# Kernel optimization log

Hardware: AMD Instinct MI355X
Metric: run time of the kernel (lower is better)

Reference implementation:

```python
import jax, jax.numpy as jnp
import numpy as np

B, C, H, W = 2, 512, 48, 48
HEADS = 8
REDUCTION = 4
DPH = max(C // REDUCTION // HEADS, 1)   # 16
TOTAL = DPH * HEADS                      # 128
EPS_NORM = 1e-12
EPS_BN = 1e-5


def setup_inputs() -> dict:
    key = jax.random.key(0)
    ks = jax.random.split(key, 6)
    x = jax.random.normal(ks[0], (B, C, H, W), dtype=jnp.float32)
    # 1x1 convs stored as [out_ch, in_ch] matrices
    w_qkv = jax.random.normal(ks[1], (3 * TOTAL, C), dtype=jnp.float32) * (1.0 / np.sqrt(C))
    w_out = jax.random.normal(ks[2], (C, TOTAL), dtype=jnp.float32) * (1.0 / np.sqrt(TOTAL))
    temperature = jnp.ones((HEADS, 1, 1), dtype=jnp.float32)
    bn_gamma = jnp.ones((C,), dtype=jnp.float32)
    bn_beta = jnp.zeros((C,), dtype=jnp.float32)
    return {"x": x, "w_qkv": w_qkv, "temperature": temperature,
            "w_out": w_out, "bn_gamma": bn_gamma, "bn_beta": bn_beta}


def _l2norm(t):
    # F.normalize(t, dim=-1): t / max(||t||_2, eps)
    n = jnp.sqrt(jnp.sum(t * t, axis=-1, keepdims=True))
    return t / jnp.maximum(n, EPS_NORM)


def reference(x, w_qkv, temperature, w_out, bn_gamma, bn_beta):
    b, c, h, w = x.shape
    n = h * w
    # qkv 1x1 conv: [b, 3*TOTAL, h, w]
    qkv = jnp.einsum('bchw,oc->bohw', x, w_qkv)
    q, k, v = jnp.split(qkv, 3, axis=1)
    # [b, heads, dph, n] -> [b, heads, n, dph]
    def heads_tokens(t):
        return t.reshape(b, HEADS, DPH, n).transpose(0, 1, 3, 2)
    q = _l2norm(heads_tokens(q))
    k = _l2norm(heads_tokens(k))
    v = heads_tokens(v)
    # [b, heads, n, n]
    attn = jnp.einsum('bhnd,bhmd->bhnm', q, k) * temperature[None]
    attn = jax.nn.softmax(attn, axis=-1)
    out = jnp.einsum('bhnm,bhmd->bhnd', attn, v)          # [b, heads, n, dph]
    out = out.transpose(0, 1, 3, 2).reshape(b, TOTAL, h, w)
    # project_out: 1x1 conv then BatchNorm2d (training-mode batch stats)
    out = jnp.einsum('bthw,ct->bchw', out, w_out)
    mean = jnp.mean(out, axis=(0, 2, 3))
    var = jnp.mean((out - mean[None, :, None, None]) ** 2, axis=(0, 2, 3))
    out = (out - mean[None, :, None, None]) * jax.lax.rsqrt(var + EPS_BN)[None, :, None, None]
    out = out * bn_gamma[None, :, None, None] + bn_beta[None, :, None, None]
    return out
```

## Files before the change

kernel.cpp:

```cpp
#include <hip/hip_runtime.h>

#define NB 2
#define CC 512
#define NN 2304
#define NH 8
#define DD 16
#define TT 128
#define O3 384

typedef __attribute__((ext_vector_type(4))) float f32x4;
typedef __attribute__((ext_vector_type(8))) __bf16 bf16x8;
typedef __attribute__((ext_vector_type(4))) __bf16 bf16x4;
typedef __attribute__((ext_vector_type(4))) _Float16 f16x4;
typedef __attribute__((ext_vector_type(2))) __fp16 hf16x2;

union hf2pair {
    hf16x2 h[2];
    f16x4  v;
};

#define OFF_XT 0u
#define OFF_WQ 4718592u
#define OFF_WO 5111808u
#define OFF_Q  5242880u
#define OFF_K  6422528u
#define OFF_VT 7602176u
#define OFF_AO 8781824u
#define OFF_PRE 9961472u

__global__ __launch_bounds__(256) void k0_convert(
    const float* __restrict__ x, const float* __restrict__ wqkv,
    const float* __restrict__ wout,
    __bf16* __restrict__ xT, __bf16* __restrict__ wqb, __bf16* __restrict__ wob)
{
    int bid = blockIdx.x;
    int t = threadIdx.x;
    if (bid < 576) {
        __shared__ float tile[64][65];
        int b = bid / 288, rem = bid % 288;
        int nt = rem / 8, cb = rem % 8;
        int n0 = nt * 64, c0 = cb * 64;
        int tc = t >> 6, tn = t & 63;
#pragma unroll
        for (int i = 0; i < 16; i++) {
            int cl = i * 4 + tc;
            tile[cl][tn] = x[(size_t)(b * CC + c0 + cl) * NN + n0 + tn];
        }
        __syncthreads();
#pragma unroll
        for (int i = 0; i < 16; i++) {
            int nl = i * 4 + tc;
            xT[(size_t)(b * NN + n0 + nl) * CC + c0 + tn] = (__bf16)tile[tn][nl];
        }
    } else {
        int wid = bid - 576;
        int base = wid * 256 + t;
#pragma unroll
        for (int i = 0; i < 16; i++) {
            int j = base + i * 16384;
            if (j < O3 * CC) wqb[j] = (__bf16)wqkv[j];
            else             wob[j - O3 * CC] = (__bf16)wout[j - O3 * CC];
        }
    }
}

__global__ __launch_bounds__(256) void k1_qkv(
    const __bf16* __restrict__ xT, const __bf16* __restrict__ wqb,
    _Float16* __restrict__ Q, _Float16* __restrict__ K, _Float16* __restrict__ VT)
{
    int ob = blockIdx.x, nt = blockIdx.y, b = blockIdx.z;
    int lane = threadIdx.x & 63, wave = threadIdx.x >> 6;
    int quad = lane >> 4, col = lane & 15;
    int n0 = nt * 64 + wave * 16;
    int o0 = ob * 64;

    f32x4 acc0 = {0.f,0.f,0.f,0.f}, acc1 = {0.f,0.f,0.f,0.f};
    f32x4 acc2 = {0.f,0.f,0.f,0.f}, acc3 = {0.f,0.f,0.f,0.f};

    const __bf16* arow  = xT + (size_t)(b * NN + n0 + col) * CC + quad * 8;
    const __bf16* brow0 = wqb + (size_t)(o0 + col) * CC + quad * 8;
    const __bf16* brow1 = brow0 + 16 * CC;
    const __bf16* brow2 = brow0 + 32 * CC;
    const __bf16* brow3 = brow0 + 48 * CC;

    bf16x8 a  = *(const bf16x8*)(arow);
    bf16x8 w0 = *(const bf16x8*)(brow0);
    bf16x8 w1 = *(const bf16x8*)(brow1);
    bf16x8 w2 = *(const bf16x8*)(brow2);
    bf16x8 w3 = *(const bf16x8*)(brow3);
#pragma unroll
    for (int ks = 0; ks < 16; ks++) {
        bf16x8 an, wn0, wn1, wn2, wn3;
        if (ks < 15) {
            an  = *(const bf16x8*)(arow + (ks + 1) * 32);
            wn0 = *(const bf16x8*)(brow0 + (ks + 1) * 32);
            wn1 = *(const bf16x8*)(brow1 + (ks + 1) * 32);
            wn2 = *(const bf16x8*)(brow2 + (ks + 1) * 32);
            wn3 = *(const bf16x8*)(brow3 + (ks + 1) * 32);
        }
        acc0 = __builtin_amdgcn_mfma_f32_16x16x32_bf16(a, w0, acc0, 0, 0, 0);
        acc1 = __builtin_amdgcn_mfma_f32_16x16x32_bf16(a, w1, acc1, 0, 0, 0);
        acc2 = __builtin_amdgcn_mfma_f32_16x16x32_bf16(a, w2, acc2, 0, 0, 0);
        acc3 = __builtin_amdgcn_mfma_f32_16x16x32_bf16(a, w3, acc3, 0, 0, 0);
        a = an; w0 = wn0; w1 = wn1; w2 = wn2; w3 = wn3;
    }

#pragma unroll
    for (int s = 0; s < 4; s++) {
        int oc = o0 + s * 16 + col;
        int d = oc & 15, h = (oc >> 4) & 7, kind = oc >> 7;
        f32x4 v = (s == 0) ? acc0 : (s == 1) ? acc1 : (s == 2) ? acc2 : acc3;
        if (kind < 2) {
            float ss0 = v[0] * v[0], ss1 = v[1] * v[1], ss2 = v[2] * v[2], ss3 = v[3] * v[3];
#pragma unroll
            for (int m = 1; m < 16; m <<= 1) {
                ss0 += __shfl_xor(ss0, m);
                ss1 += __shfl_xor(ss1, m);
                ss2 += __shfl_xor(ss2, m);
                ss3 += __shfl_xor(ss3, m);
            }
            v[0] *= 1.0f / fmaxf(sqrtf(ss0), 1e-12f);
            v[1] *= 1.0f / fmaxf(sqrtf(ss1), 1e-12f);
            v[2] *= 1.0f / fmaxf(sqrtf(ss2), 1e-12f);
            v[3] *= 1.0f / fmaxf(sqrtf(ss3), 1e-12f);
            _Float16* dst = (kind == 0 ? Q : K) + (size_t)(b * NH + h) * NN * DD;
#pragma unroll
            for (int r = 0; r < 4; r++) {
                int n = n0 + quad * 4 + r;
                dst[(size_t)n * DD + d] = (_Float16)v[r];
            }
        } else {
            f16x4 pk;
#pragma unroll
            for (int r = 0; r < 4; r++) pk[r] = (_Float16)v[r];
            int n = n0 + quad * 4;
            *(f16x4*)(VT + (size_t)((b * NH + h) * DD + d) * NN + n) = pk;
        }
    }
}

__global__ __launch_bounds__(512) void k2_attn(
    const _Float16* __restrict__ Q, const _Float16* __restrict__ K,
    const _Float16* __restrict__ VT, const float* __restrict__ temp,
    __bf16* __restrict__ AO)
{
    __shared__ float Osh[8][16][64];
    __shared__ float Lsh[8][64];

    int qt = blockIdx.x, bh = blockIdx.y;
    int lane = threadIdx.x & 63, wave = threadIdx.x >> 6;
    int quad = lane >> 4, col = lane & 15;
    int kbase = wave * 288;
    int qbase = qt * 64;

    const _Float16* Qb = Q + (size_t)bh * NN * DD;
    float tl2 = temp[bh & 7] * 1.4426950408889634f;
    _Float16 tl2h = (_Float16)tl2;

    f16x4 qf0 = *(const f16x4*)(Qb + (size_t)(qbase +  0 + col) * DD + quad * 4);
    f16x4 qf1 = *(const f16x4*)(Qb + (size_t)(qbase + 16 + col) * DD + quad * 4);
    f16x4 qf2 = *(const f16x4*)(Qb + (size_t)(qbase + 32 + col) * DD + quad * 4);
    f16x4 qf3 = *(const f16x4*)(Qb + (size_t)(qbase + 48 + col) * DD + quad * 4);
#pragma unroll
    for (int j = 0; j < 4; j++) {
        qf0[j] *= tl2h; qf1[j] *= tl2h; qf2[j] *= tl2h; qf3[j] *= tl2h;
    }
    const f16x4 onesf = {(_Float16)1.f, (_Float16)1.f, (_Float16)1.f, (_Float16)1.f};

    f32x4 oa0 = {0.f,0.f,0.f,0.f}, oa1 = {0.f,0.f,0.f,0.f};
    f32x4 oa2 = {0.f,0.f,0.f,0.f}, oa3 = {0.f,0.f,0.f,0.f};
    f32x4 lc0 = {0.f,0.f,0.f,0.f}, lc1 = {0.f,0.f,0.f,0.f};
    f32x4 lc2 = {0.f,0.f,0.f,0.f}, lc3 = {0.f,0.f,0.f,0.f};
    const f32x4 zc = {0.f,0.f,0.f,0.f};

    const _Float16* kp = K + (size_t)bh * NN * DD + (size_t)(kbase + col) * DD + quad * 4;
    const _Float16* vp = VT + (size_t)bh * DD * NN + (size_t)col * NN + kbase + quad * 4;

    f16x4 kfa = *(const f16x4*)(kp);
    f16x4 kfb = *(const f16x4*)(kp + 16 * DD);
    f16x4 vfa = *(const f16x4*)(vp);
    f16x4 vfb = *(const f16x4*)(vp + 16);

#define K2_CHUNK(KF, VF)                                                        \
    {                                                                           \
        f32x4 s0 = __builtin_amdgcn_mfma_f32_16x16x16f16(KF, qf0, zc, 0, 0, 0); \
        f32x4 s1 = __builtin_amdgcn_mfma_f32_16x16x16f16(KF, qf1, zc, 0, 0, 0); \
        f32x4 s2 = __builtin_amdgcn_mfma_f32_16x16x16f16(KF, qf2, zc, 0, 0, 0); \
        f32x4 s3 = __builtin_amdgcn_mfma_f32_16x16x16f16(KF, qf3, zc, 0, 0, 0); \
        hf2pair u0, u1, u2, u3;                                                 \
        u0.h[0] = __builtin_amdgcn_cvt_pkrtz(__builtin_amdgcn_exp2f(s0[0]),     \
                                             __builtin_amdgcn_exp2f(s0[1]));    \
        u0.h[1] = __builtin_amdgcn_cvt_pkrtz(__builtin_amdgcn_exp2f(s0[2]),     \
                                             __builtin_amdgcn_exp2f(s0[3]));    \
        u1.h[0] = __builtin_amdgcn_cvt_pkrtz(__builtin_amdgcn_exp2f(s1[0]),     \
                                             __builtin_amdgcn_exp2f(s1[1]));    \
        u1.h[1] = __builtin_amdgcn_cvt_pkrtz(__builtin_amdgcn_exp2f(s1[2]),     \
                                             __builtin_amdgcn_exp2f(s1[3]));    \
        u2.h[0] = __builtin_amdgcn_cvt_pkrtz(__builtin_amdgcn_exp2f(s2[0]),     \
                                             __builtin_amdgcn_exp2f(s2[1]));    \
        u2.h[1] = __builtin_amdgcn_cvt_pkrtz(__builtin_amdgcn_exp2f(s2[2]),     \
                                             __builtin_amdgcn_exp2f(s2[3]));    \
        u3.h[0] = __builtin_amdgcn_cvt_pkrtz(__builtin_amdgcn_exp2f(s3[0]),     \
                                             __builtin_amdgcn_exp2f(s3[1]));    \
        u3.h[1] = __builtin_amdgcn_cvt_pkrtz(__builtin_amdgcn_exp2f(s3[2]),     \
                                             __builtin_amdgcn_exp2f(s3[3]));    \
        f16x4 p0 = u0.v, p1 = u1.v, p2 = u2.v, p3 = u3.v;                       \
        lc0 = __builtin_amdgcn_mfma_f32_16x16x16f16(onesf, p0, lc0, 0, 0, 0);   \
        lc1 = __builtin_amdgcn_mfma_f32_16x16x16f16(onesf, p1, lc1, 0, 0, 0);   \
        lc2 = __builtin_amdgcn_mfma_f32_16x16x16f16(onesf, p2, lc2, 0, 0, 0);   \
        lc3 = __builtin_amdgcn_mfma_f32_16x16x16f16(onesf, p3, lc3, 0, 0, 0);   \
        oa0 = __builtin_amdgcn_mfma_f32_16x16x16f16(VF, p0, oa0, 0, 0, 0);      \
        oa1 = __builtin_amdgcn_mfma_f32_16x16x16f16(VF, p1, oa1, 0, 0, 0);      \
        oa2 = __builtin_amdgcn_mfma_f32_16x16x16f16(VF, p2, oa2, 0, 0, 0);      \
        oa3 = __builtin_amdgcn_mfma_f32_16x16x16f16(VF, p3, oa3, 0, 0, 0);      \
    }

    for (int g = 0; g < 9; ++g) {
        f16x4 kna, knb, vna, vnb;
        if (g < 8) {
            kna = *(const f16x4*)(kp + 32 * DD);
            knb = *(const f16x4*)(kp + 48 * DD);
            vna = *(const f16x4*)(vp + 32);
            vnb = *(const f16x4*)(vp + 48);
        }
        K2_CHUNK(kfa, vfa)
        K2_CHUNK(kfb, vfb)
        kfa = kna; kfb = knb; vfa = vna; vfb = vnb;
        kp += 32 * DD; vp += 32;
    }
#undef K2_CHUNK

#pragma unroll
    for (int r = 0; r < 4; ++r) {
        Osh[wave][quad * 4 + r][ 0 + col] = oa0[r];
        Osh[wave][quad * 4 + r][16 + col] = oa1[r];
        Osh[wave][quad * 4 + r][32 + col] = oa2[r];
        Osh[wave][quad * 4 + r][48 + col] = oa3[r];
    }
    float lv = (quad == 0) ? lc0[0] : (quad == 1) ? lc1[0] : (quad == 2) ? lc2[0] : lc3[0];
    Lsh[wave][quad * 16 + col] = lv;
    __syncthreads();

    int t = threadIdx.x;
    int q = t & 63, dg = t >> 6;
    float l = 0.f;
#pragma unroll
    for (int w = 0; w < 8; ++w) l += Lsh[w][q];
    float inv = 1.0f / l;
    float o0 = 0.f, o1 = 0.f;
#pragma unroll
    for (int w = 0; w < 8; ++w) {
        o0 += Osh[w][dg * 2 + 0][q];
        o1 += Osh[w][dg * 2 + 1][q];
    }
    int b = bh >> 3, h = bh & 7;
    __bf16* dst = AO + (size_t)(b * NN + qbase + q) * TT + h * DD + dg * 2;
    dst[0] = (__bf16)(o0 * inv);
    dst[1] = (__bf16)(o1 * inv);
}

__global__ __launch_bounds__(256) void k3_proj(
    const __bf16* __restrict__ AO, const __bf16* __restrict__ wob,
    __bf16* __restrict__ pre)
{
    int cb = blockIdx.x, nt = blockIdx.y, b = blockIdx.z;
    int lane = threadIdx.x & 63, wave = threadIdx.x >> 6;
    int quad = lane >> 4, col = lane & 15;
    int n0 = nt * 64 + wave * 16, c0 = cb * 32;

    f32x4 acc0 = {0.f, 0.f, 0.f, 0.f};
    f32x4 acc1 = {0.f, 0.f, 0.f, 0.f};

    const __bf16* ab = AO + (size_t)(b * NN + n0 + col) * TT + quad * 8;
    const __bf16* wb0 = wob + (size_t)(c0 + col) * TT + quad * 8;
    const __bf16* wb1 = wb0 + 16 * TT;
#pragma unroll
    for (int ks = 0; ks < 4; ks++) {
        bf16x8 a  = *(const bf16x8*)(ab + ks * 32);
        bf16x8 w0 = *(const bf16x8*)(wb0 + ks * 32);
        bf16x8 w1 = *(const bf16x8*)(wb1 + ks * 32);
        acc0 = __builtin_amdgcn_mfma_f32_16x16x32_bf16(a, w0, acc0, 0, 0, 0);
        acc1 = __builtin_amdgcn_mfma_f32_16x16x32_bf16(a, w1, acc1, 0, 0, 0);
    }
#pragma unroll
    for (int s = 0; s < 2; s++) {
        int c = c0 + s * 16 + col;
        f32x4 v = (s == 0) ? acc0 : acc1;
        bf16x4 pk;
        pk[0] = (__bf16)v[0]; pk[1] = (__bf16)v[1];
        pk[2] = (__bf16)v[2]; pk[3] = (__bf16)v[3];
        *(bf16x4*)(pre + (size_t)(b * CC + c) * NN + n0 + quad * 4) = pk;
    }
}

__global__ __launch_bounds__(256) void k4_bn(
    const __bf16* __restrict__ pre, float* __restrict__ out,
    const float* __restrict__ gamma, const float* __restrict__ beta)
{
    int c = blockIdx.x;
    int t = threadIdx.x;
    float vals[18];
    float s = 0.f, q = 0.f;
#pragma unroll
    for (int i = 0; i < 18; i++) {
        int j = i * 256 + t;
        int b = j / NN, n = j % NN;
        float v = (float)pre[(size_t)(b * CC + c) * NN + n];
        vals[i] = v; s += v; q += v * v;
    }
#pragma unroll
    for (int m = 1; m < 64; m <<= 1) { s += __shfl_xor(s, m); q += __shfl_xor(q, m); }
    __shared__ float rs[4], rq[4];
    int lane = t & 63, wave = t >> 6;
    if (lane == 0) { rs[wave] = s; rq[wave] = q; }
    __syncthreads();
    s = rs[0] + rs[1] + rs[2] + rs[3];
    q = rq[0] + rq[1] + rq[2] + rq[3];
    float mean = s * (1.0f / 4608.0f);
    float var = q * (1.0f / 4608.0f) - mean * mean;
    float sc = rsqrtf(var + 1e-5f) * gamma[c];
    float sh = beta[c] - mean * sc;
#pragma unroll
    for (int i = 0; i < 18; i++) {
        int j = i * 256 + t;
        int b = j / NN, n = j % NN;
        out[(size_t)(b * CC + c) * NN + n] = vals[i] * sc + sh;
    }
}

extern "C" void kernel_launch(void* const* d_in, const int* in_sizes, int n_in,
                              void* d_out, int out_size, void* d_ws, size_t ws_size,
                              hipStream_t stream) {
    const float* x     = (const float*)d_in[0];
    const float* wqkv  = (const float*)d_in[1];
    const float* temp  = (const float*)d_in[2];
    const float* wout  = (const float*)d_in[3];
    const float* gamma = (const float*)d_in[4];
    const float* beta  = (const float*)d_in[5];
    float* out = (float*)d_out;
    char* ws = (char*)d_ws;

    __bf16* xT  = (__bf16*)(ws + OFF_XT);
    __bf16* wqb = (__bf16*)(ws + OFF_WQ);
    __bf16* wob = (__bf16*)(ws + OFF_WO);
    _Float16* Q  = (_Float16*)(ws + OFF_Q);
    _Float16* K  = (_Float16*)(ws + OFF_K);
    _Float16* VT = (_Float16*)(ws + OFF_VT);
    __bf16* AO  = (__bf16*)(ws + OFF_AO);
    __bf16* PRE = (__bf16*)(ws + OFF_PRE);

    k0_convert<<<640, 256, 0, stream>>>(x, wqkv, wout, xT, wqb, wob);
    k1_qkv<<<dim3(6, 36, 2), 256, 0, stream>>>(xT, wqb, Q, K, VT);
    k2_attn<<<dim3(36, 16), 512, 0, stream>>>(Q, K, VT, temp, AO);
    k3_proj<<<dim3(16, 36, 2), 256, 0, stream>>>(AO, wob, PRE);
    k4_bn<<<512, 256, 0, stream>>>(PRE, out, gamma, beta);
}
```

Baseline: 131.5 us.

## Vectorize memory accesses across kernels and replace ones-MFMA row sums with VALU adds

The convert kernel now uses float4 loads and packed bf16x4 stores for both the x transpose and the weight casts. The attention kernel drops the four extra MFMAs that computed softmax denominators against a ones vector. It sums the exp values in fp32 registers instead, reduced with cross-quad shuffles, and writes its output as packed bf16 pairs. The BN kernel uses vectorized bf16x4 loads and float4 stores. Together these aim to cut memory transaction count and matrix-unit work in the attention loop, at the cost of extra VALU adds and LDS bank conflicts in the new transpose pattern.

Measured after the change: 127.7 us, median of 2. 1.03x faster.

```diff
diff --git a/kernel.cpp b/kernel.cpp
--- a/kernel.cpp
+++ b/kernel.cpp
@@ -11,6 +11,7 @@
 typedef __attribute__((ext_vector_type(4))) float f32x4;
 typedef __attribute__((ext_vector_type(8))) __bf16 bf16x8;
 typedef __attribute__((ext_vector_type(4))) __bf16 bf16x4;
+typedef __attribute__((ext_vector_type(2))) __bf16 bf16x2;
 typedef __attribute__((ext_vector_type(4))) _Float16 f16x4;
 typedef __attribute__((ext_vector_type(2))) __fp16 hf16x2;
 
@@ -40,26 +41,43 @@
         int b = bid / 288, rem = bid % 288;
         int nt = rem / 8, cb = rem % 8;
         int n0 = nt * 64, c0 = cb * 64;
-        int tc = t >> 6, tn = t & 63;
-#pragma unroll
-        for (int i = 0; i < 16; i++) {
-            int cl = i * 4 + tc;
-            tile[cl][tn] = x[(size_t)(b * CC + c0 + cl) * NN + n0 + tn];
+        int nq = (t & 15) * 4;
+        int cs = t >> 4;
+#pragma unroll
+        for (int i = 0; i < 4; i++) {
+            int c = i * 16 + cs;
+            f32x4 v = *(const f32x4*)(x + (size_t)(b * CC + c0 + c) * NN + n0 + nq);
+            tile[c][nq + 0] = v[0];
+            tile[c][nq + 1] = v[1];
+            tile[c][nq + 2] = v[2];
+            tile[c][nq + 3] = v[3];
         }
         __syncthreads();
-#pragma unroll
-        for (int i = 0; i < 16; i++) {
-            int nl = i * 4 + tc;
-            xT[(size_t)(b * NN + n0 + nl) * CC + c0 + tn] = (__bf16)tile[tn][nl];
+        int cq = (t & 15) * 4;
+        int ns = t >> 4;
+#pragma unroll
+        for (int i = 0; i < 4; i++) {
+            int n = i * 16 + ns;
+            bf16x4 pk;
+            pk[0] = (__bf16)tile[cq + 0][n];
+            pk[1] = (__bf16)tile[cq + 1][n];
+            pk[2] = (__bf16)tile[cq + 2][n];
+            pk[3] = (__bf16)tile[cq + 3][n];
+            *(bf16x4*)(xT + (size_t)(b * NN + n0 + n) * CC + c0 + cq) = pk;
         }
     } else {
         int wid = bid - 576;
-        int base = wid * 256 + t;
-#pragma unroll
-        for (int i = 0; i < 16; i++) {
-            int j = base + i * 16384;
-            if (j < O3 * CC) wqb[j] = (__bf16)wqkv[j];
-            else             wob[j - O3 * CC] = (__bf16)wout[j - O3 * CC];
+#pragma unroll
+        for (int i = 0; i < 4; i++) {
+            int jq = wid * 256 + t + i * 16384;
+            int j = jq * 4;
+            f32x4 v = (j < O3 * CC) ? *(const f32x4*)(wqkv + j)
+                                    : *(const f32x4*)(wout + (j - O3 * CC));
+            bf16x4 pk;
+            pk[0] = (__bf16)v[0]; pk[1] = (__bf16)v[1];
+            pk[2] = (__bf16)v[2]; pk[3] = (__bf16)v[3];
+            if (j < O3 * CC) *(bf16x4*)(wqb + j) = pk;
+            else             *(bf16x4*)(wob + (j - O3 * CC)) = pk;
         }
     }
 }
@@ -165,12 +183,10 @@
     for (int j = 0; j < 4; j++) {
         qf0[j] *= tl2h; qf1[j] *= tl2h; qf2[j] *= tl2h; qf3[j] *= tl2h;
     }
-    const f16x4 onesf = {(_Float16)1.f, (_Float16)1.f, (_Float16)1.f, (_Float16)1.f};
 
     f32x4 oa0 = {0.f,0.f,0.f,0.f}, oa1 = {0.f,0.f,0.f,0.f};
     f32x4 oa2 = {0.f,0.f,0.f,0.f}, oa3 = {0.f,0.f,0.f,0.f};
-    f32x4 lc0 = {0.f,0.f,0.f,0.f}, lc1 = {0.f,0.f,0.f,0.f};
-    f32x4 lc2 = {0.f,0.f,0.f,0.f}, lc3 = {0.f,0.f,0.f,0.f};
+    float la0 = 0.f, la1 = 0.f, la2 = 0.f, la3 = 0.f;
     const f32x4 zc = {0.f,0.f,0.f,0.f};
 
     const _Float16* kp = K + (size_t)bh * NN * DD + (size_t)(kbase + col) * DD + quad * 4;
@@ -187,32 +203,31 @@
         f32x4 s1 = __builtin_amdgcn_mfma_f32_16x16x16f16(KF, qf1, zc, 0, 0, 0); \
         f32x4 s2 = __builtin_amdgcn_mfma_f32_16x16x16f16(KF, qf2, zc, 0, 0, 0); \
         f32x4 s3 = __builtin_amdgcn_mfma_f32_16x16x16f16(KF, qf3, zc, 0, 0, 0); \
+        float e00 = __builtin_amdgcn_exp2f(s0[0]), e01 = __builtin_amdgcn_exp2f(s0[1]); \
+        float e02 = __builtin_amdgcn_exp2f(s0[2]), e03 = __builtin_amdgcn_exp2f(s0[3]); \
+        float e10 = __builtin_amdgcn_exp2f(s1[0]), e11 = __builtin_amdgcn_exp2f(s1[1]); \
+        float e12 = __builtin_amdgcn_exp2f(s1[2]), e13 = __builtin_amdgcn_exp2f(s1[3]); \
+        float e20 = __builtin_amdgcn_exp2f(s2[0]), e21 = __builtin_amdgcn_exp2f(s2[1]); \
+        float e22 = __builtin_amdgcn_exp2f(s2[2]), e23 = __builtin_amdgcn_exp2f(s2[3]); \
+        float e30 = __builtin_amdgcn_exp2f(s3[0]), e31 = __builtin_amdgcn_exp2f(s3[1]); \
+        float e32 = __builtin_amdgcn_exp2f(s3[2]), e33 = __builtin_amdgcn_exp2f(s3[3]); \
+        la0 += (e00 + e01) + (e02 + e03);                                       \
+        la1 += (e10 + e11) + (e12 + e13);                                       \
+        la2 += (e20 + e21) + (e22 + e23);                                       \
+        la3 += (e30 + e31) + (e32 + e33);                                       \
         hf2pair u0, u1, u2, u3;                                                 \
-        u0.h[0] = __builtin_amdgcn_cvt_pkrtz(__builtin_amdgcn_exp2f(s0[0]),     \
-                                             __builtin_amdgcn_exp2f(s0[1]));    \
-        u0.h[1] = __builtin_amdgcn_cvt_pkrtz(__builtin_amdgcn_exp2f(s0[2]),     \
-                                             __builtin_amdgcn_exp2f(s0[3]));    \
-        u1.h[0] = __builtin_amdgcn_cvt_pkrtz(__builtin_amdgcn_exp2f(s1[0]),     \
-                                             __builtin_amdgcn_exp2f(s1[1]));    \
-        u1.h[1] = __builtin_amdgcn_cvt_pkrtz(__builtin_amdgcn_exp2f(s1[2]),     \
-                                             __builtin_amdgcn_exp2f(s1[3]));    \
-        u2.h[0] = __builtin_amdgcn_cvt_pkrtz(__builtin_amdgcn_exp2f(s2[0]),     \
-                                             __builtin_amdgcn_exp2f(s2[1]));    \
-        u2.h[1] = __builtin_amdgcn_cvt_pkrtz(__builtin_amdgcn_exp2f(s2[2]),     \
-                                             __builtin_amdgcn_exp2f(s2[3]));    \
-        u3.h[0] = __builtin_amdgcn_cvt_pkrtz(__builtin_amdgcn_exp2f(s3[0]),     \
-                                             __builtin_amdgcn_exp2f(s3[1]));    \
-        u3.h[1] = __builtin_amdgcn_cvt_pkrtz(__builtin_amdgcn_exp2f(s3[2]),     \
-                                             __builtin_amdgcn_exp2f(s3[3]));    \
-        f16x4 p0 = u0.v, p1 = u1.v, p2 = u2.v, p3 = u3.v;                       \
-        lc0 = __builtin_amdgcn_mfma_f32_16x16x16f16(onesf, p0, lc0, 0, 0, 0);   \
-        lc1 = __builtin_amdgcn_mfma_f32_16x16x16f16(onesf, p1, lc1, 0, 0, 0);   \
-        lc2 = __builtin_amdgcn_mfma_f32_16x16x16f16(onesf, p2, lc2, 0, 0, 0);   \
-        lc3 = __builtin_amdgcn_mfma_f32_16x16x16f16(onesf, p3, lc3, 0, 0, 0);   \
-        oa0 = __builtin_amdgcn_mfma_f32_16x16x16f16(VF, p0, oa0, 0, 0, 0);      \
-        oa1 = __builtin_amdgcn_mfma_f32_16x16x16f16(VF, p1, oa1, 0, 0, 0);      \
-        oa2 = __builtin_amdgcn_mfma_f32_16x16x16f16(VF, p2, oa2, 0, 0, 0);      \
-        oa3 = __builtin_amdgcn_mfma_f32_16x16x16f16(VF, p3, oa3, 0, 0, 0);      \
+        u0.h[0] = __builtin_amdgcn_cvt_pkrtz(e00, e01);                         \
+        u0.h[1] = __builtin_amdgcn_cvt_pkrtz(e02, e03);                         \
+        u1.h[0] = __builtin_amdgcn_cvt_pkrtz(e10, e11);                         \
+        u1.h[1] = __builtin_amdgcn_cvt_pkrtz(e12, e13);                         \
+        u2.h[0] = __builtin_amdgcn_cvt_pkrtz(e20, e21);                         \
+        u2.h[1] = __builtin_amdgcn_cvt_pkrtz(e22, e23);                         \
+        u3.h[0] = __builtin_amdgcn_cvt_pkrtz(e30, e31);                         \
+        u3.h[1] = __builtin_amdgcn_cvt_pkrtz(e32, e33);                         \
+        oa0 = __builtin_amdgcn_mfma_f32_16x16x16f16(VF, u0.v, oa0, 0, 0, 0);    \
+        oa1 = __builtin_amdgcn_mfma_f32_16x16x16f16(VF, u1.v, oa1, 0, 0, 0);    \
+        oa2 = __builtin_amdgcn_mfma_f32_16x16x16f16(VF, u2.v, oa2, 0, 0, 0);    \
+        oa3 = __builtin_amdgcn_mfma_f32_16x16x16f16(VF, u3.v, oa3, 0, 0, 0);    \
     }
 
     for (int g = 0; g < 9; ++g) {
@@ -230,6 +245,11 @@
     }
 #undef K2_CHUNK
 
+    la0 += __shfl_xor(la0, 16); la0 += __shfl_xor(la0, 32);
+    la1 += __shfl_xor(la1, 16); la1 += __shfl_xor(la1, 32);
+    la2 += __shfl_xor(la2, 16); la2 += __shfl_xor(la2, 32);
+    la3 += __shfl_xor(la3, 16); la3 += __shfl_xor(la3, 32);
+
 #pragma unroll
     for (int r = 0; r < 4; ++r) {
         Osh[wave][quad * 4 + r][ 0 + col] = oa0[r];
@@ -237,7 +257,7 @@
         Osh[wave][quad * 4 + r][32 + col] = oa2[r];
         Osh[wave][quad * 4 + r][48 + col] = oa3[r];
     }
-    float lv = (quad == 0) ? lc0[0] : (quad == 1) ? lc1[0] : (quad == 2) ? lc2[0] : lc3[0];
+    float lv = (quad == 0) ? la0 : (quad == 1) ? la1 : (quad == 2) ? la2 : la3;
     Lsh[wave][quad * 16 + col] = lv;
     __syncthreads();
 
@@ -254,9 +274,10 @@
         o1 += Osh[w][dg * 2 + 1][q];
     }
     int b = bh >> 3, h = bh & 7;
-    __bf16* dst = AO + (size_t)(b * NN + qbase + q) * TT + h * DD + dg * 2;
-    dst[0] = (__bf16)(o0 * inv);
-    dst[1] = (__bf16)(o1 * inv);
+    bf16x2 pk;
+    pk[0] = (__bf16)(o0 * inv);
+    pk[1] = (__bf16)(o1 * inv);
+    *(bf16x2*)(AO + (size_t)(b * NN + qbase + q) * TT + h * DD + dg * 2) = pk;
 }
 
 __global__ __launch_bounds__(256) void k3_proj(
@@ -299,14 +320,22 @@
 {
     int c = blockIdx.x;
     int t = threadIdx.x;
-    float vals[18];
+    float vals[2][9];
     float s = 0.f, q = 0.f;
 #pragma unroll
-    for (int i = 0; i < 18; i++) {
-        int j = i * 256 + t;
-        int b = j / NN, n = j % NN;
-        float v = (float)pre[(size_t)(b * CC + c) * NN + n];
-        vals[i] = v; s += v; q += v * v;
+    for (int b = 0; b < 2; b++) {
+        const __bf16* base = pre + (size_t)(b * CC + c) * NN;
+#pragma unroll
+        for (int r = 0; r < 2; r++) {
+            bf16x4 x4 = *(const bf16x4*)(base + r * 1024 + t * 4);
+#pragma unroll
+            for (int j = 0; j < 4; j++) {
+                float v = (float)x4[j];
+                vals[b][r * 4 + j] = v; s += v; q += v * v;
+            }
+        }
+        float v = (float)base[2048 + t];
+        vals[b][8] = v; s += v; q += v * v;
     }
 #pragma unroll
     for (int m = 1; m < 64; m <<= 1) { s += __shfl_xor(s, m); q += __shfl_xor(q, m); }
@@ -321,10 +350,16 @@
     float sc = rsqrtf(var + 1e-5f) * gamma[c];
     float sh = beta[c] - mean * sc;
 #pragma unroll
-    for (int i = 0; i < 18; i++) {
-        int j = i * 256 + t;
-        int b = j / NN, n = j % NN;
-        out[(size_t)(b * CC + c) * NN + n] = vals[i] * sc + sh;
+    for (int b = 0; b < 2; b++) {
+        float* obase = out + (size_t)(b * CC + c) * NN;
+#pragma unroll
+        for (int r = 0; r < 2; r++) {
+            f32x4 o;
+#pragma unroll
+            for (int j = 0; j < 4; j++) o[j] = vals[b][r * 4 + j] * sc + sh;
+            *(f32x4*)(obase + r * 1024 + t * 4) = o;
+        }
+        obase[2048 + t] = vals[b][8] * sc + sh;
     }
 }
 
```
